# Kernel tuning notes

Hardware: AMD Instinct MI355X
Metric: run time of the kernel (lower is better)

The kernel has to match this reference:

```python
import jax, jax.numpy as jnp
import numpy as np

B, NLOC, F, H = 16384, 12, 512, 256

def setup_inputs() -> dict:
    key = jax.random.key(0)
    ks = jax.random.split(key, 8)
    s = lambda n: 1.0 / np.sqrt(n)
    return {
        "global_feature": jax.random.normal(ks[0], (B, F), jnp.float32),
        "local_features": jax.random.normal(ks[1], (B, NLOC, F), jnp.float32),
        "Wq": jax.random.normal(ks[2], (F, H), jnp.float32) * s(F),
        "bq": jnp.zeros((H,), jnp.float32),
        "Wk": jax.random.normal(ks[3], (F, H), jnp.float32) * s(F),
        "bk": jnp.zeros((H,), jnp.float32),
        "Wv": jax.random.normal(ks[4], (F, H), jnp.float32) * s(F),
        "bv": jnp.zeros((H,), jnp.float32),
        "w_dr": jax.random.normal(ks[5], (NLOC,), jnp.float32) * s(NLOC),  # Linear(12,1) weight
        "b_dr": jnp.zeros((), jnp.float32),
        "Wf": jax.random.normal(ks[6], (2 * H, F), jnp.float32) * s(2 * H),
        "bf": jnp.zeros((F,), jnp.float32),
    }

def reference(global_feature, local_features, Wq, bq, Wk, bk, Wv, bv, w_dr, b_dr, Wf, bf):
    scale = 1.0 / jnp.sqrt(jnp.float32(H))
    # dimension_reduction over the 12 local tokens: Linear(12 -> 1)
    lf_mean = jnp.einsum('bkf,k->bf', local_features, w_dr) + b_dr  # [B, F]
    # --- local queries attend to the single global token ---
    gk = global_feature @ Wk + bk                       # [B, H]
    gv = global_feature @ Wv + bv                       # [B, H]
    lq = local_features @ Wq + bq                       # [B, 12, H]
    s1 = (jnp.einsum('bkh,bh->bk', lq, gk) * scale)[..., None]  # [B, 12, 1]
    a1 = jax.nn.softmax(s1, axis=-1)                    # softmax over length-1 key axis
    weighted_global = a1 * gv[:, None, :]               # [B, 12, H]
    # --- global query attends over the 12 local tokens ---
    gq = global_feature @ Wq + bq                       # [B, H]
    lk = local_features @ Wk + bk                       # [B, 12, H]
    lv = local_features @ Wv + bv                       # [B, 12, H]
    s2 = jnp.einsum('bh,bkh->bk', gq, lk) * scale       # [B, 12]
    a2 = jax.nn.softmax(s2, axis=-1)
    local_to_global = jnp.einsum('bk,bkh->bh', a2, lv)  # [B, H]
    # pool the 12-token axis of the weighted global feature
    wg_mean = jnp.einsum('bkh,k->bh', weighted_global, w_dr) + b_dr  # [B, H]
    combined = jnp.concatenate([local_to_global, wg_mean], axis=-1)  # [B, 2H]
    fused = jax.nn.relu(combined @ Wf + bf) + lf_mean + global_feature  # [B, F]
    return fused
```

## Files before the change

### kernel.cpp

```cpp
#include <hip/hip_runtime.h>

#define NLOC 12
#define F_DIM 512
#define H_DIM 256

typedef float f4 __attribute__((ext_vector_type(4)));
typedef _Float16 half4 __attribute__((ext_vector_type(4)));
typedef _Float16 half8 __attribute__((ext_vector_type(8)));

#define OFF_W1   0ul
#define OFF_W2   (OFF_W1 + 512ul*512*2)
#define OFF_C1   (OFF_W2 + 512ul*1024*2)
#define OFF_CVEC (OFF_C1 + 2048ul)
#define OFF_ACAT (OFF_CVEC + 2048ul)
#define OFF_BASE (OFF_ACAT + 16384ul*1024*2)

__global__ void __launch_bounds__(256) precompute_w(
    const float* __restrict__ Wq, const float* __restrict__ Wk,
    const float* __restrict__ Wv, const float* __restrict__ Wf,
    const float* __restrict__ wdr, const float* __restrict__ bq,
    const float* __restrict__ bv, const float* __restrict__ bdr,
    const float* __restrict__ bfv,
    _Float16* __restrict__ W1, _Float16* __restrict__ W2,
    float* __restrict__ c1, float* __restrict__ cvec)
{
    const int mode = blockIdx.z;
    const int t = threadIdx.x;

    if (mode == 3) {
        if (blockIdx.y != 0 || blockIdx.x >= 2) return;
        const int f = blockIdx.x * 256 + t;
        f4 a = {0.f, 0.f, 0.f, 0.f};
        const f4* wk4 = (const f4*)(Wk + (long)f * H_DIM);
        const f4* bq4 = (const f4*)bq;
#pragma unroll 4
        for (int h4 = 0; h4 < H_DIM / 4; ++h4) a += wk4[h4] * bq4[h4];
        c1[f] = a[0] + a[1] + a[2] + a[3];

        float s1 = 0.f, s2 = 0.f, s3 = 0.f;
#pragma unroll 4
        for (int h = 0; h < H_DIM; ++h) {
            float w1v = Wf[h * F_DIM + f];
            float w2v = Wf[(H_DIM + h) * F_DIM + f];
            float bvh = bv[h];
            s1 += bvh * w1v; s2 += bvh * w2v; s3 += w2v;
        }
        float S = 0.f;
#pragma unroll
        for (int k = 0; k < NLOC; ++k) S += wdr[k];
        cvec[f] = s1 + S * s2 + bdr[0] * s3 + bfv[f];
        return;
    }

    __shared__ float X[32][264];
    __shared__ float Y[32][264];
    const int f0 = blockIdx.x * 32;
    const int j0 = blockIdx.y * 32;

    {
        const int r = t >> 3, cb = (t & 7) * 32;
        const float* ysrc = ((mode == 0) ? Wq : Wv) + (j0 + r) * H_DIM + cb;
#pragma unroll
        for (int u = 0; u < 32; u += 4)
            *(f4*)&Y[r][cb + u] = *(const f4*)(ysrc + u);
        if (mode == 0) {
            const float* xsrc = Wk + (f0 + r) * H_DIM + cb;
#pragma unroll
            for (int u = 0; u < 32; u += 4)
                *(f4*)&X[r][cb + u] = *(const f4*)(xsrc + u);
        }
    }
    if (mode != 0) {
        const int h = t;
        const int hoff = (mode == 2) ? H_DIM : 0;
        const float* xsrc = Wf + (long)(h + hoff) * F_DIM + f0;
        f4 v[8];
#pragma unroll
        for (int u = 0; u < 8; ++u) v[u] = *(const f4*)(xsrc + u * 4);
#pragma unroll
        for (int r = 0; r < 32; ++r) X[r][h] = v[r >> 2][r & 3];
    }
    __syncthreads();

    const int fy = t >> 4, jx = t & 15;
    float a00 = 0.f, a01 = 0.f, a10 = 0.f, a11 = 0.f;
#pragma unroll 8
    for (int h = 0; h < H_DIM; ++h) {
        float x0 = X[fy][h], x1 = X[fy + 16][h];
        float y0 = Y[jx][h], y1 = Y[jx + 16][h];
        a00 += x0 * y0; a01 += x0 * y1; a10 += x1 * y0; a11 += x1 * y1;
    }
    if (mode == 2) {
        float S = 0.f;
#pragma unroll
        for (int k = 0; k < NLOC; ++k) S += wdr[k];
        a00 *= S; a01 *= S; a10 *= S; a11 *= S;
    }
    if (mode == 0) {
        W1[(f0 + fy) * F_DIM + (j0 + jx)]             = (_Float16)a00;
        W1[(f0 + fy) * F_DIM + (j0 + jx + 16)]        = (_Float16)a01;
        W1[(f0 + fy + 16) * F_DIM + (j0 + jx)]        = (_Float16)a10;
        W1[(f0 + fy + 16) * F_DIM + (j0 + jx + 16)]   = (_Float16)a11;
    } else {
        const long co = (mode == 2) ? F_DIM : 0;
        W2[(long)(f0 + fy) * 1024 + co + (j0 + jx)]           = (_Float16)a00;
        W2[(long)(f0 + fy) * 1024 + co + (j0 + jx + 16)]      = (_Float16)a01;
        W2[(long)(f0 + fy + 16) * 1024 + co + (j0 + jx)]      = (_Float16)a10;
        W2[(long)(f0 + fy + 16) * 1024 + co + (j0 + jx + 16)] = (_Float16)a11;
    }
}

__global__ void __launch_bounds__(256, 2) fused_local(
    const float* __restrict__ g, const float* __restrict__ loc,
    const _Float16* __restrict__ W1, const float* __restrict__ c1,
    const float* __restrict__ wdr, const float* __restrict__ bdr,
    _Float16* __restrict__ Acat, _Float16* __restrict__ base)
{
    __shared__ _Float16 G[32][520];
    __shared__ _Float16 T[32][520];
    const int tid = threadIdx.x;
    const int lane = tid & 63;
    const int wave = tid >> 6;
    const int quad = lane >> 4;
    const int l16 = lane & 15;
    const long m0 = (long)blockIdx.x * 32;

    {
        const int r = tid >> 3;
        const int cb = (tid & 7) * 8;
#pragma unroll
        for (int u = 0; u < 512; u += 64) {
            const float* src = g + (m0 + r) * F_DIM + cb + u;
            f4 v0 = *(const f4*)(src);
            f4 v1 = *(const f4*)(src + 4);
            half8 hv;
#pragma unroll
            for (int j = 0; j < 4; ++j) { hv[j] = (_Float16)v0[j]; hv[4 + j] = (_Float16)v1[j]; }
            *(half8*)&G[r][cb + u] = hv;
            *(half8*)(Acat + (m0 + r) * 1024 + 512 + cb + u) = hv;
        }
    }
    __syncthreads();

    const int wn1 = wave * 32;
    for (int nt = 0; nt < 4; ++nt) {
        const int n0 = nt * 128;
        const _Float16* wb0 = W1 + (long)(n0 + wn1 + l16) * F_DIM + quad * 8;
        const _Float16* wb1 = wb0 + 16 * F_DIM;
        f4 acc[2][2] = {{{0.f,0.f,0.f,0.f},{0.f,0.f,0.f,0.f}},
                        {{0.f,0.f,0.f,0.f},{0.f,0.f,0.f,0.f}}};
#pragma unroll
        for (int k0 = 0; k0 < 512; k0 += 32) {
            half8 b0 = *(const half8*)(wb0 + k0);
            half8 b1 = *(const half8*)(wb1 + k0);
            half8 a0 = *(const half8*)&G[l16][k0 + quad * 8];
            half8 a1 = *(const half8*)&G[16 + l16][k0 + quad * 8];
            acc[0][0] = __builtin_amdgcn_mfma_f32_16x16x32_f16(a0, b0, acc[0][0], 0, 0, 0);
            acc[0][1] = __builtin_amdgcn_mfma_f32_16x16x32_f16(a0, b1, acc[0][1], 0, 0, 0);
            acc[1][0] = __builtin_amdgcn_mfma_f32_16x16x32_f16(a1, b0, acc[1][0], 0, 0, 0);
            acc[1][1] = __builtin_amdgcn_mfma_f32_16x16x32_f16(a1, b1, acc[1][1], 0, 0, 0);
        }
#pragma unroll
        for (int ni = 0; ni < 2; ++ni) {
            const int col = n0 + wn1 + ni * 16 + l16;
            const float cv = c1[col];
#pragma unroll
            for (int mi = 0; mi < 2; ++mi)
#pragma unroll
                for (int i = 0; i < 4; ++i)
                    T[mi * 16 + quad * 4 + i][col] = (_Float16)(acc[mi][ni][i] + cv);
        }
    }

    const int c0 = lane * 4;
    const int c1i = 256 + lane * 4;
    const float bd = bdr[0];
    float wv[NLOC];
#pragma unroll
    for (int k = 0; k < NLOC; ++k) wv[k] = wdr[k];

    f4 laA[NLOC], laB[NLOC];
    {
        const float* lb0 = loc + (m0 + wave * 8) * (NLOC * F_DIM);
#pragma unroll
        for (int k = 0; k < NLOC; ++k) laA[k] = *(const f4*)(lb0 + k * F_DIM + c0);
    }
    __syncthreads();

    auto row_body = [&](int rr, f4 (&la)[NLOC], f4 (&laN)[NLOC]) {
        const int bl = wave * 8 + rr;
        const long b = m0 + bl;
        const float* lb = loc + b * (NLOC * F_DIM);

        f4 lbv[NLOC];
#pragma unroll
        for (int k = 0; k < NLOC; ++k)
            lbv[k] = *(const f4*)(lb + k * F_DIM + c1i);
        if (rr < 7) {
            const float* lbn = lb + NLOC * F_DIM;
#pragma unroll
            for (int k = 0; k < NLOC; ++k)
                laN[k] = *(const f4*)(lbn + k * F_DIM + c0);
        }

        f4 taf = __builtin_convertvector(*(const half4*)&T[bl][c0], f4);
        f4 tbf = __builtin_convertvector(*(const half4*)&T[bl][c1i], f4);

        float p[NLOC];
#pragma unroll
        for (int k = 0; k < NLOC; ++k) {
            f4 prod = la[k] * taf + lbv[k] * tbf;
            p[k] = prod[0] + prod[1] + prod[2] + prod[3];
        }
#pragma unroll
        for (int k = 0; k < NLOC; ++k) {
            float v = p[k];
            v += __shfl_xor(v, 1);
            v += __shfl_xor(v, 2);
            v += __shfl_xor(v, 4);
            v += __shfl_xor(v, 8);
            v += __shfl_xor(v, 16);
            v += __shfl_xor(v, 32);
            p[k] = v * 0.0625f;
        }
        float mx = p[0];
#pragma unroll
        for (int k = 1; k < NLOC; ++k) mx = fmaxf(mx, p[k]);
        float e[NLOC], s = 0.f;
#pragma unroll
        for (int k = 0; k < NLOC; ++k) { e[k] = expf(p[k] - mx); s += e[k]; }
        const float inv = 1.f / s;

        f4 pA = {0.f,0.f,0.f,0.f}, pB = {0.f,0.f,0.f,0.f};
        f4 fA = {0.f,0.f,0.f,0.f}, fB = {0.f,0.f,0.f,0.f};
#pragma unroll
        for (int k = 0; k < NLOC; ++k) {
            const float ak = e[k] * inv;
            const float wk = wv[k];
            pA += ak * la[k]; pB += ak * lbv[k];
            fA += wk * la[k]; fB += wk * lbv[k];
        }
        half4 gA = *(const half4*)&G[bl][c0];
        half4 gB = *(const half4*)&G[bl][c1i];
        fA += bd + __builtin_convertvector(gA, f4);
        fB += bd + __builtin_convertvector(gB, f4);

        *(half4*)(Acat + b * 1024 + c0)          = __builtin_convertvector(pA, half4);
        *(half4*)(Acat + b * 1024 + c1i)         = __builtin_convertvector(pB, half4);
        *(half4*)(base + b * F_DIM + c0)         = __builtin_convertvector(fA, half4);
        *(half4*)(base + b * F_DIM + c1i)        = __builtin_convertvector(fB, half4);
    };

#pragma unroll
    for (int it = 0; it < 4; ++it) {
        row_body(it * 2,     laA, laB);
        row_body(it * 2 + 1, laB, laA);
    }
}

__global__ void __launch_bounds__(256, 2) gemm_final(
    const _Float16* __restrict__ A, const _Float16* __restrict__ Bt,
    const float* __restrict__ cvec, const _Float16* __restrict__ base,
    float* __restrict__ out)
{
    __shared__ _Float16 As[2][128][40];
    __shared__ _Float16 Bs[2][128][40];
    const int tid = threadIdx.x;
    const int lane = tid & 63;
    const int wave = tid >> 6;
    const int quad = lane >> 4;
    const int l16 = lane & 15;
    const int wm = (wave & 1) * 64;
    const int wn = (wave >> 1) * 64;
    const long m0 = (long)blockIdx.x * 128;
    const int n0 = blockIdx.y * 128;
    const int sr = tid >> 1, sc = (tid & 1) * 16;

    const _Float16* ap = A  + (m0 + sr) * 1024 + sc;
    const _Float16* bp = Bt + (long)(n0 + sr) * 1024 + sc;

    f4 acc[4][4];
#pragma unroll
    for (int mi = 0; mi < 4; ++mi)
#pragma unroll
        for (int nj = 0; nj < 4; ++nj) acc[mi][nj] = (f4){0.f,0.f,0.f,0.f};

    {
        uint4 a0 = *(const uint4*)(ap);
        uint4 a1 = *(const uint4*)(ap + 8);
        uint4 b0 = *(const uint4*)(bp);
        uint4 b1 = *(const uint4*)(bp + 8);
        *(uint4*)&As[0][sr][sc]     = a0;
        *(uint4*)&As[0][sr][sc + 8] = a1;
        *(uint4*)&Bs[0][sr][sc]     = b0;
        *(uint4*)&Bs[0][sr][sc + 8] = b1;
    }
    __syncthreads();

#pragma unroll 4
    for (int kt = 0; kt < 32; ++kt) {
        const int cur = kt & 1;
        uint4 a0, a1, b0, b1;
        if (kt < 31) {
            const int k0 = (kt + 1) * 32;
            a0 = *(const uint4*)(ap + k0);
            a1 = *(const uint4*)(ap + k0 + 8);
            b0 = *(const uint4*)(bp + k0);
            b1 = *(const uint4*)(bp + k0 + 8);
        }
        half8 af[4], bf[4];
#pragma unroll
        for (int i = 0; i < 4; ++i) {
            af[i] = *(const half8*)&As[cur][wm + i * 16 + l16][quad * 8];
            bf[i] = *(const half8*)&Bs[cur][wn + i * 16 + l16][quad * 8];
        }
#pragma unroll
        for (int mi = 0; mi < 4; ++mi)
#pragma unroll
            for (int nj = 0; nj < 4; ++nj)
                acc[mi][nj] = __builtin_amdgcn_mfma_f32_16x16x32_f16(af[mi], bf[nj], acc[mi][nj], 0, 0, 0);
        if (kt < 31) {
            *(uint4*)&As[cur ^ 1][sr][sc]     = a0;
            *(uint4*)&As[cur ^ 1][sr][sc + 8] = a1;
            *(uint4*)&Bs[cur ^ 1][sr][sc]     = b0;
            *(uint4*)&Bs[cur ^ 1][sr][sc + 8] = b1;
        }
        __syncthreads();
    }

#pragma unroll
    for (int mi = 0; mi < 4; ++mi)
#pragma unroll
        for (int nj = 0; nj < 4; ++nj) {
            const int col = n0 + wn + nj * 16 + l16;
            const float cv = cvec[col];
#pragma unroll
            for (int i = 0; i < 4; ++i) {
                const long row = m0 + wm + mi * 16 + quad * 4 + i;
                float v = acc[mi][nj][i] + cv;
                v = fmaxf(v, 0.f) + (float)base[row * F_DIM + col];
                out[row * F_DIM + col] = v;
            }
        }
}

extern "C" void kernel_launch(void* const* d_in, const int* in_sizes, int n_in,
                              void* d_out, int out_size, void* d_ws, size_t ws_size,
                              hipStream_t stream)
{
    (void)in_sizes; (void)n_in; (void)out_size; (void)ws_size;
    const float* gf  = (const float*)d_in[0];
    const float* loc = (const float*)d_in[1];
    const float* Wq  = (const float*)d_in[2];
    const float* bq  = (const float*)d_in[3];
    const float* Wk  = (const float*)d_in[4];
    const float* Wv  = (const float*)d_in[6];
    const float* bv  = (const float*)d_in[7];
    const float* wdr = (const float*)d_in[8];
    const float* bdr = (const float*)d_in[9];
    const float* Wf  = (const float*)d_in[10];
    const float* bfv = (const float*)d_in[11];
    float* out = (float*)d_out;

    char* ws = (char*)d_ws;
    _Float16* W1   = (_Float16*)(ws + OFF_W1);
    _Float16* W2   = (_Float16*)(ws + OFF_W2);
    float*    c1   = (float*)(ws + OFF_C1);
    float*    cvec = (float*)(ws + OFF_CVEC);
    _Float16* Acat = (_Float16*)(ws + OFF_ACAT);
    _Float16* base = (_Float16*)(ws + OFF_BASE);

    precompute_w<<<dim3(16, 16, 4), 256, 0, stream>>>(
        Wq, Wk, Wv, Wf, wdr, bq, bv, bdr, bfv, W1, W2, c1, cvec);
    fused_local<<<512, 256, 0, stream>>>(gf, loc, W1, c1, wdr, bdr, Acat, base);
    gemm_final<<<dim3(128, 4), 256, 0, stream>>>(Acat, W2, cvec, base, out);
}
```

Before: 679.5 us.

## Fuse final GEMM into local attention kernel, keep intermediates in LDS

Merges the second kernel (final projection GEMM with ReLU and residual) into the local attention kernel. Each 32-row block now keeps its pooled attention output and global features in shared memory and runs the 32x512x1024 GEMM directly against W2 from global memory. The residual base is held in registers and staged through LDS for the epilogue. This removes the round trip of the Acat and base intermediates through HBM and one kernel launch. In exchange, W2 operands are read straight from global/L2 by every block with no LDS tiling, and register pressure rises from the 16 accumulators plus the saved base values.

```diff
diff --git a/kernel.cpp b/kernel.cpp
--- a/kernel.cpp
+++ b/kernel.cpp
@@ -12,8 +12,6 @@
 #define OFF_W2   (OFF_W1 + 512ul*512*2)
 #define OFF_C1   (OFF_W2 + 512ul*1024*2)
 #define OFF_CVEC (OFF_C1 + 2048ul)
-#define OFF_ACAT (OFF_CVEC + 2048ul)
-#define OFF_BASE (OFF_ACAT + 16384ul*1024*2)
 
 __global__ void __launch_bounds__(256) precompute_w(
     const float* __restrict__ Wq, const float* __restrict__ Wk,
@@ -110,11 +108,12 @@
     }
 }
 
-__global__ void __launch_bounds__(256, 2) fused_local(
+__global__ void __launch_bounds__(256, 2) fused_all(
     const float* __restrict__ g, const float* __restrict__ loc,
-    const _Float16* __restrict__ W1, const float* __restrict__ c1,
+    const _Float16* __restrict__ W1, const _Float16* __restrict__ W2,
+    const float* __restrict__ c1, const float* __restrict__ cvec,
     const float* __restrict__ wdr, const float* __restrict__ bdr,
-    _Float16* __restrict__ Acat, _Float16* __restrict__ base)
+    float* __restrict__ out)
 {
     __shared__ _Float16 G[32][520];
     __shared__ _Float16 T[32][520];
@@ -137,7 +136,6 @@
 #pragma unroll
             for (int j = 0; j < 4; ++j) { hv[j] = (_Float16)v0[j]; hv[4 + j] = (_Float16)v1[j]; }
             *(half8*)&G[r][cb + u] = hv;
-            *(half8*)(Acat + (m0 + r) * 1024 + 512 + cb + u) = hv;
         }
     }
     __syncthreads();
@@ -179,6 +177,8 @@
 #pragma unroll
     for (int k = 0; k < NLOC; ++k) wv[k] = wdr[k];
 
+    half4 bhA[8], bhB[8];
+
     f4 laA[NLOC], laB[NLOC];
     {
         const float* lb0 = loc + (m0 + wave * 8) * (NLOC * F_DIM);
@@ -245,10 +245,10 @@
         fA += bd + __builtin_convertvector(gA, f4);
         fB += bd + __builtin_convertvector(gB, f4);
 
-        *(half4*)(Acat + b * 1024 + c0)          = __builtin_convertvector(pA, half4);
-        *(half4*)(Acat + b * 1024 + c1i)         = __builtin_convertvector(pB, half4);
-        *(half4*)(base + b * F_DIM + c0)         = __builtin_convertvector(fA, half4);
-        *(half4*)(base + b * F_DIM + c1i)        = __builtin_convertvector(fB, half4);
+        *(half4*)&T[bl][c0]  = __builtin_convertvector(pA, half4);
+        *(half4*)&T[bl][c1i] = __builtin_convertvector(pB, half4);
+        bhA[rr] = __builtin_convertvector(fA, half4);
+        bhB[rr] = __builtin_convertvector(fB, half4);
     };
 
 #pragma unroll
@@ -256,92 +256,64 @@
         row_body(it * 2,     laA, laB);
         row_body(it * 2 + 1, laB, laA);
     }
-}
-
-__global__ void __launch_bounds__(256, 2) gemm_final(
-    const _Float16* __restrict__ A, const _Float16* __restrict__ Bt,
-    const float* __restrict__ cvec, const _Float16* __restrict__ base,
-    float* __restrict__ out)
-{
-    __shared__ _Float16 As[2][128][40];
-    __shared__ _Float16 Bs[2][128][40];
-    const int tid = threadIdx.x;
-    const int lane = tid & 63;
-    const int wave = tid >> 6;
-    const int quad = lane >> 4;
-    const int l16 = lane & 15;
-    const int wm = (wave & 1) * 64;
-    const int wn = (wave >> 1) * 64;
-    const long m0 = (long)blockIdx.x * 128;
-    const int n0 = blockIdx.y * 128;
-    const int sr = tid >> 1, sc = (tid & 1) * 16;
-
-    const _Float16* ap = A  + (m0 + sr) * 1024 + sc;
-    const _Float16* bp = Bt + (long)(n0 + sr) * 1024 + sc;
-
-    f4 acc[4][4];
-#pragma unroll
-    for (int mi = 0; mi < 4; ++mi)
-#pragma unroll
-        for (int nj = 0; nj < 4; ++nj) acc[mi][nj] = (f4){0.f,0.f,0.f,0.f};
-
-    {
-        uint4 a0 = *(const uint4*)(ap);
-        uint4 a1 = *(const uint4*)(ap + 8);
-        uint4 b0 = *(const uint4*)(bp);
-        uint4 b1 = *(const uint4*)(bp + 8);
-        *(uint4*)&As[0][sr][sc]     = a0;
-        *(uint4*)&As[0][sr][sc + 8] = a1;
-        *(uint4*)&Bs[0][sr][sc]     = b0;
-        *(uint4*)&Bs[0][sr][sc + 8] = b1;
-    }
-    __syncthreads();
+    __syncthreads();
+
+    const int wn = wave * 128;
+    f4 acc[2][8];
+#pragma unroll
+    for (int mi = 0; mi < 2; ++mi)
+#pragma unroll
+        for (int nj = 0; nj < 8; ++nj) acc[mi][nj] = (f4){0.f,0.f,0.f,0.f};
+
+    const _Float16* w2w = W2 + (long)(wn + l16) * 1024 + quad * 8;
 
 #pragma unroll 4
-    for (int kt = 0; kt < 32; ++kt) {
-        const int cur = kt & 1;
-        uint4 a0, a1, b0, b1;
-        if (kt < 31) {
-            const int k0 = (kt + 1) * 32;
-            a0 = *(const uint4*)(ap + k0);
-            a1 = *(const uint4*)(ap + k0 + 8);
-            b0 = *(const uint4*)(bp + k0);
-            b1 = *(const uint4*)(bp + k0 + 8);
-        }
-        half8 af[4], bf[4];
-#pragma unroll
-        for (int i = 0; i < 4; ++i) {
-            af[i] = *(const half8*)&As[cur][wm + i * 16 + l16][quad * 8];
-            bf[i] = *(const half8*)&Bs[cur][wn + i * 16 + l16][quad * 8];
-        }
-#pragma unroll
-        for (int mi = 0; mi < 4; ++mi)
-#pragma unroll
-            for (int nj = 0; nj < 4; ++nj)
-                acc[mi][nj] = __builtin_amdgcn_mfma_f32_16x16x32_f16(af[mi], bf[nj], acc[mi][nj], 0, 0, 0);
-        if (kt < 31) {
-            *(uint4*)&As[cur ^ 1][sr][sc]     = a0;
-            *(uint4*)&As[cur ^ 1][sr][sc + 8] = a1;
-            *(uint4*)&Bs[cur ^ 1][sr][sc]     = b0;
-            *(uint4*)&Bs[cur ^ 1][sr][sc + 8] = b1;
-        }
-        __syncthreads();
-    }
-
-#pragma unroll
-    for (int mi = 0; mi < 4; ++mi)
-#pragma unroll
-        for (int nj = 0; nj < 4; ++nj) {
-            const int col = n0 + wn + nj * 16 + l16;
-            const float cv = cvec[col];
+    for (int kt = 0; kt < 16; ++kt) {
+        const int k0 = kt * 32;
+        half8 a0 = *(const half8*)&T[l16][k0 + quad * 8];
+        half8 a1 = *(const half8*)&T[16 + l16][k0 + quad * 8];
+#pragma unroll
+        for (int nj = 0; nj < 8; ++nj) {
+            half8 b = *(const half8*)(w2w + nj * 16 * 1024 + k0);
+            acc[0][nj] = __builtin_amdgcn_mfma_f32_16x16x32_f16(a0, b, acc[0][nj], 0, 0, 0);
+            acc[1][nj] = __builtin_amdgcn_mfma_f32_16x16x32_f16(a1, b, acc[1][nj], 0, 0, 0);
+        }
+    }
+#pragma unroll 4
+    for (int kt = 0; kt < 16; ++kt) {
+        const int k0 = kt * 32;
+        half8 a0 = *(const half8*)&G[l16][k0 + quad * 8];
+        half8 a1 = *(const half8*)&G[16 + l16][k0 + quad * 8];
+#pragma unroll
+        for (int nj = 0; nj < 8; ++nj) {
+            half8 b = *(const half8*)(w2w + nj * 16 * 1024 + 512 + k0);
+            acc[0][nj] = __builtin_amdgcn_mfma_f32_16x16x32_f16(a0, b, acc[0][nj], 0, 0, 0);
+            acc[1][nj] = __builtin_amdgcn_mfma_f32_16x16x32_f16(a1, b, acc[1][nj], 0, 0, 0);
+        }
+    }
+
+    __syncthreads();
+#pragma unroll
+    for (int rr = 0; rr < 8; ++rr) {
+        const int bl = wave * 8 + rr;
+        *(half4*)&T[bl][c0]  = bhA[rr];
+        *(half4*)&T[bl][c1i] = bhB[rr];
+    }
+    __syncthreads();
+
+#pragma unroll
+    for (int nj = 0; nj < 8; ++nj) {
+        const int col = wn + nj * 16 + l16;
+        const float cv = cvec[col];
+#pragma unroll
+        for (int mi = 0; mi < 2; ++mi)
 #pragma unroll
             for (int i = 0; i < 4; ++i) {
-                const long row = m0 + wm + mi * 16 + quad * 4 + i;
-                float v = acc[mi][nj][i] + cv;
-                v = fmaxf(v, 0.f) + (float)base[row * F_DIM + col];
-                out[row * F_DIM + col] = v;
+                const int rl = mi * 16 + quad * 4 + i;
+                float v = fmaxf(acc[mi][nj][i] + cv, 0.f) + (float)T[rl][col];
+                out[(m0 + rl) * F_DIM + col] = v;
             }
-        }
+    }
 }
 
 extern "C" void kernel_launch(void* const* d_in, const int* in_sizes, int n_in,
@@ -367,11 +339,9 @@
     _Float16* W2   = (_Float16*)(ws + OFF_W2);
     float*    c1   = (float*)(ws + OFF_C1);
     float*    cvec = (float*)(ws + OFF_CVEC);
-    _Float16* Acat = (_Float16*)(ws + OFF_ACAT);
-    _Float16* base = (_Float16*)(ws + OFF_BASE);
 
     precompute_w<<<dim3(16, 16, 4), 256, 0, stream>>>(
         Wq, Wk, Wv, Wf, wdr, bq, bv, bdr, bfv, W1, W2, c1, cvec);
-    fused_local<<<512, 256, 0, stream>>>(gf, loc, W1, c1, wdr, bdr, Acat, base);
-    gemm_final<<<dim3(128, 4), 256, 0, stream>>>(Acat, W2, cvec, base, out);
+    fused_all<<<512, 256, 0, stream>>>(
+        gf, loc, W1, W2, c1, cvec, wdr, bdr, out);
 }
```

Result: slower. 877.9 us (+29.2%).
